# Kernel tuning notes

Measured on AMD Instinct MI355X. Metric: run time of the kernel, lower is better.

Reference implementation:

```python
import jax, jax.numpy as jnp
import numpy as np


def _dwconv(x, w, pad):
    # depthwise conv, NCHW, weight (C,1,kh,kw), feature_group_count=C
    return jax.lax.conv_general_dilated(
        x, w, window_strides=(1, 1), padding=pad,
        feature_group_count=x.shape[1],
        dimension_numbers=('NCHW', 'OIHW', 'NCHW'))


def _max_channel_relu(x):
    # assumed MaxChannelReLU: keep only the channel-max value at each (b,h,w)
    return x * (x == jnp.max(x, axis=1, keepdims=True))


def setup_inputs() -> dict:
    key = jax.random.key(0)
    ks = jax.random.split(key, 6)
    B, C, H, W = 16, 64, 128, 128
    x = jax.random.normal(ks[0], (B, C, H, W), dtype=jnp.float32)
    w_bbx = 0.1 * jax.random.normal(ks[1], (C, 1, 1, 1), dtype=jnp.float32)
    w_width = 0.1 * jax.random.normal(ks[2], (C, 1, 1, 11), dtype=jnp.float32)
    w_width_sh = 0.1 * jax.random.normal(ks[3], (C, 1, 1, 1), dtype=jnp.float32)
    w_height = 0.1 * jax.random.normal(ks[4], (C, 1, 11, 1), dtype=jnp.float32)
    w_height_sh = 0.1 * jax.random.normal(ks[5], (C, 1, 1, 1), dtype=jnp.float32)
    return {"x": x, "w_bbx": w_bbx, "w_width": w_width,
            "w_width_sh": w_width_sh, "w_height": w_height,
            "w_height_sh": w_height_sh}


def reference(x, w_bbx, w_width, w_width_sh, w_height, w_height_sh):
    B, C, H, W = x.shape
    # self.bbx: depthwise 1x1 conv == per-channel scale
    wh = x * w_bbx.reshape(1, C, 1, 1)
    # width branch: depthwise (1,11) conv pad 5, scaled by W, then shared 1x1
    w = _dwconv(wh, w_width, [(0, 0), (5, 5)]) * W
    w = w * w_width_sh.reshape(1, C, 1, 1)
    # height branch: depthwise (11,1) conv pad 5, scaled by H, then shared 1x1
    h = _dwconv(wh, w_height, [(5, 5), (0, 0)]) * H
    h = h * w_height_sh.reshape(1, C, 1, 1)
    sx = jax.nn.sigmoid(x)
    M = jnp.max(sx, axis=(-2, -1), keepdims=True) - 0.01
    score = x * (sx > M).astype(x.dtype)
    S = jnp.sum(score, axis=(-2, -1), keepdims=True)
    sn = score / S  # normalized weights, reused by all weighted reductions
    ws = jnp.sum(w * sn, axis=(-2, -1))
    hs = jnp.sum(h * sn, axis=(-2, -1))
    ps = jnp.max(sx, axis=(-2, -1))
    col = jnp.arange(W, dtype=x.dtype).reshape(1, 1, 1, W)
    row = jnp.arange(H, dtype=x.dtype).reshape(1, 1, H, 1)
    x1 = jnp.sum(col * sn, axis=(-2, -1)) - ws / 2
    y1 = jnp.sum(row * sn, axis=(-2, -1)) - hs / 2
    x2 = x1 + ws
    y2 = y1 + hs
    score_m = _max_channel_relu(score)
    w_m = _max_channel_relu(w)
    h_m = _max_channel_relu(h)
    i = jnp.broadcast_to(jnp.arange(B, dtype=x.dtype)[:, None], (B, C))
    bbox = jnp.stack([i, x1, y1, x2, y2, ps], axis=-1).reshape(-1, 6)
    return jnp.concatenate([score_m, w_m, h_m], axis=1), bbox
```

## Files before the change

kernel.cpp:

```cpp
#include <hip/hip_runtime.h>
#include <math.h>

#define BATCH 16
#define CH    64
#define HH    128
#define WW    128
#define PLANE (HH*WW)
#define OUT0  (BATCH*3*CH*PLANE)
#define SR4    36
#define TSROWS 18
#define PART_OFF 2048
#define MB_OFF   90112
#define MB_N     786432


__device__ __forceinline__ unsigned enc32(float f) {
    unsigned u = __float_as_uint(f);
    return (u & 0x80000000u) ? ~u : (u | 0x80000000u);
}
__device__ __forceinline__ float dec32(unsigned k) {
    unsigned u = (k & 0x80000000u) ? (k ^ 0x80000000u) : ~k;
    return __uint_as_float(u);
}

__global__ __launch_bounds__(256) void k_max(const float* __restrict__ x,
                                             float* __restrict__ ws) {
    int bid = blockIdx.x;
    int tid = threadIdx.x;
    const float4* xp = (const float4*)(x + (size_t)bid * PLANE);
    float m = -INFINITY;
#pragma unroll
    for (int i = 0; i < 16; i++) {
        float4 v = xp[i * 256 + tid];
        m = fmaxf(m, fmaxf(fmaxf(v.x, v.y), fmaxf(v.z, v.w)));
    }
#pragma unroll
    for (int off = 32; off; off >>= 1) m = fmaxf(m, __shfl_xor(m, off, 64));
    __shared__ float sm[4];
    int wid = tid >> 6, lane = tid & 63;
    if (lane == 0) sm[wid] = m;
    __syncthreads();
    if (tid == 0) {
        float mm = fmaxf(fmaxf(sm[0], sm[1]), fmaxf(sm[2], sm[3]));
        float ps = 1.0f / (1.0f + expf(-mm));
        ws[bid] = ps - 0.01f;
        ws[1024 + bid] = ps;
    }
}

template <int CPG>
__global__ __launch_bounds__(256) void k_conv(
    const float* __restrict__ x,
    const float* __restrict__ w_bbx, const float* __restrict__ w_width,
    const float* __restrict__ w_width_sh, const float* __restrict__ w_height,
    const float* __restrict__ w_height_sh,
    const float* __restrict__ ws, float* __restrict__ wsums,
    unsigned long long* __restrict__ mb) {
    __shared__ float4 xs4[2][TSROWS * SR4];
    __shared__ float red[CPG * 4 * 5];
    int t = blockIdx.x;
    int g = blockIdx.y;
    int b = blockIdx.z;
    int tid = threadIdx.x;
    int r = tid >> 5, q = tid & 31;
    int wid = tid >> 6, lane = tid & 63;

    for (int j = tid; j < 2 * TSROWS * SR4; j += 256)
        ((float4*)xs4)[j] = make_float4(0.f, 0.f, 0.f, 0.f);
    __syncthreads();
    int cbase = g * CPG;
    {
        const float* xp = x + (size_t)(b * 64 + cbase) * PLANE;
        for (int j = tid; j < TSROWS * 32; j += 256) {
            int i = j >> 5, c4 = j & 31;
            int gr = t * 8 - 5 + i;
            float4 v = make_float4(0.f, 0.f, 0.f, 0.f);
            if ((unsigned)gr < 128u) v = ((const float4*)xp)[gr * 32 + c4];
            xs4[0][i * SR4 + 2 + c4] = v;
        }
    }
    unsigned long long kW[4], kH[4], kS[4];
#pragma unroll
    for (int j = 0; j < 4; j++) { kW[j] = 0ull; kH[j] = 0ull; kS[j] = 0ull; }

    int cur = 0;
    for (int cc = 0; cc < CPG; cc++) {
        __syncthreads();
        int c = cbase + cc;
        float4 p0 = make_float4(0.f, 0.f, 0.f, 0.f);
        float4 p1 = make_float4(0.f, 0.f, 0.f, 0.f);
        float4 p2 = make_float4(0.f, 0.f, 0.f, 0.f);
        bool have = (cc + 1 < CPG);
        if (have) {
            const float* xp = x + (size_t)(b * 64 + c + 1) * PLANE;
            int i0 = tid >> 5, c4 = tid & 31;
            int g0 = t * 8 - 5 + i0;
            if ((unsigned)g0 < 128u) p0 = ((const float4*)xp)[g0 * 32 + c4];
            int g1 = g0 + 8;
            if ((unsigned)g1 < 128u) p1 = ((const float4*)xp)[g1 * 32 + c4];
            if (tid < 64) {
                int g2 = g0 + 16;
                if ((unsigned)g2 < 128u) p2 = ((const float4*)xp)[g2 * 32 + c4];
            }
        }
        float wkc[11], hkc[11];
#pragma unroll
        for (int k = 0; k < 11; k++) {
            wkc[k] = w_width[c * 11 + k];
            hkc[k] = w_height[c * 11 + k];
        }
        float cb = w_bbx[c];
        float cw = 128.0f * w_width_sh[c] * cb;
        float chs = 128.0f * w_height_sh[c] * cb;
        float M = ws[b * 64 + c];

        float4 vx;
        float hx = 0.f, hy = 0.f, hz = 0.f, hw = 0.f;
#pragma unroll
        for (int k = 0; k < 11; k++) {
            float4 v = xs4[cur][(r + k) * SR4 + 2 + q];
            if (k == 5) vx = v;
            hx += v.x * hkc[k]; hy += v.y * hkc[k];
            hz += v.z * hkc[k]; hw += v.w * hkc[k];
        }
        float wbuf[20];
        {
            float4 a0 = xs4[cur][(r + 5) * SR4 + q + 0];
            float4 a1 = xs4[cur][(r + 5) * SR4 + q + 1];
            float4 a3 = xs4[cur][(r + 5) * SR4 + q + 3];
            float4 a4 = xs4[cur][(r + 5) * SR4 + q + 4];
            wbuf[0] = a0.x;  wbuf[1] = a0.y;  wbuf[2] = a0.z;  wbuf[3] = a0.w;
            wbuf[4] = a1.x;  wbuf[5] = a1.y;  wbuf[6] = a1.z;  wbuf[7] = a1.w;
            wbuf[8] = vx.x;  wbuf[9] = vx.y;  wbuf[10] = vx.z; wbuf[11] = vx.w;
            wbuf[12] = a3.x; wbuf[13] = a3.y; wbuf[14] = a3.z; wbuf[15] = a3.w;
            wbuf[16] = a4.x; wbuf[17] = a4.y; wbuf[18] = a4.z; wbuf[19] = a4.w;
        }
        float wo[4];
#pragma unroll
        for (int j = 0; j < 4; j++) {
            float acc = 0.f;
#pragma unroll
            for (int k = 0; k < 11; k++) acc += wbuf[j + 3 + k] * wkc[k];
            wo[j] = acc * cw;
        }
        float ho[4] = {hx * chs, hy * chs, hz * chs, hw * chs};
        float xv[4] = {vx.x, vx.y, vx.z, vx.w};
        float S = 0.f, Sw = 0.f, Sh = 0.f, Scol = 0.f, Srow = 0.f;
#pragma unroll
        for (int j = 0; j < 4; j++) {
            float sx = 1.0f / (1.0f + expf(-xv[j]));
            float sc = (sx > M) ? xv[j] : 0.0f;
            S += sc;
            Sw += wo[j] * sc;
            Sh += ho[j] * sc;
            Scol += (float)(4 * q + j) * sc;
            unsigned long long cand;
            cand = ((unsigned long long)enc32(sc) << 32) | (unsigned)c;
            if (cand > kS[j]) kS[j] = cand;
            cand = ((unsigned long long)enc32(wo[j]) << 32) | (unsigned)c;
            if (cand > kW[j]) kW[j] = cand;
            cand = ((unsigned long long)enc32(ho[j]) << 32) | (unsigned)c;
            if (cand > kH[j]) kH[j] = cand;
        }
        Srow = (float)(t * 8 + r) * S;
#pragma unroll
        for (int off = 32; off; off >>= 1) {
            S    += __shfl_xor(S, off, 64);
            Sw   += __shfl_xor(Sw, off, 64);
            Sh   += __shfl_xor(Sh, off, 64);
            Scol += __shfl_xor(Scol, off, 64);
            Srow += __shfl_xor(Srow, off, 64);
        }
        if (lane == 0) {
            float* rr = &red[(cc * 4 + wid) * 5];
            rr[0] = S; rr[1] = Sw; rr[2] = Sh; rr[3] = Scol; rr[4] = Srow;
        }
        if (have) {
            int i0 = tid >> 5, c4 = tid & 31;
            xs4[cur ^ 1][i0 * SR4 + 2 + c4] = p0;
            xs4[cur ^ 1][(i0 + 8) * SR4 + 2 + c4] = p1;
            if (tid < 64) xs4[cur ^ 1][(i0 + 16) * SR4 + 2 + c4] = p2;
        }
        cur ^= 1;
    }
    __syncthreads();
    if (tid < CPG * 5) {
        int cc = tid / 5, j = tid % 5;
        float s = red[(cc * 4 + 0) * 5 + j] + red[(cc * 4 + 1) * 5 + j]
                + red[(cc * 4 + 2) * 5 + j] + red[(cc * 4 + 3) * 5 + j];
        int c = cbase + cc;
        wsums[(((size_t)(b * 64 + c)) * 16 + t) * 5 + j] = s;
    }
    int gr = t * 8 + r;
    size_t pix = (size_t)gr * 128 + 4 * q;
    unsigned long long* o = mb + (size_t)g * MB_N;
    size_t i0 = (size_t)(b * 3 + 0) * 16384 + pix;
    size_t i1 = (size_t)(b * 3 + 1) * 16384 + pix;
    size_t i2 = (size_t)(b * 3 + 2) * 16384 + pix;
#pragma unroll
    for (int j = 0; j < 4; j++) {
        o[i0 + j] = kS[j];
        o[i1 + j] = kW[j];
        o[i2 + j] = kH[j];
    }
}

template <int NG>
__global__ __launch_bounds__(256) void k_scatter(
    const unsigned long long* __restrict__ mb, float* __restrict__ out) {
    int chunk = blockIdx.x;
    int f = blockIdx.y;
    int b = blockIdx.z;
    int tid = threadIdx.x;
    size_t pix = (size_t)chunk * 1024 + tid * 4;
    size_t ki = (size_t)(b * 3 + f) * 16384 + pix;
    float val[4];
    int win[4];
#pragma unroll
    for (int j = 0; j < 4; j++) {
        unsigned long long k = 0ull;
#pragma unroll
        for (int g2 = 0; g2 < NG; g2++) {
            unsigned long long kg = mb[(size_t)g2 * MB_N + ki + j];
            if (kg > k) k = kg;
        }
        val[j] = dec32((unsigned)(k >> 32));
        win[j] = (int)(k & 63u);
    }
    float* ob = out + (size_t)(b * 192 + f * 64) * PLANE + pix;
#pragma unroll
    for (int c = 0; c < 64; c++) {
        float4 o;
        o.x = (win[0] == c) ? val[0] : 0.f;
        o.y = (win[1] == c) ? val[1] : 0.f;
        o.z = (win[2] == c) ? val[2] : 0.f;
        o.w = (win[3] == c) ? val[3] : 0.f;
        *(float4*)&ob[(size_t)c * PLANE] = o;
    }
}

__global__ __launch_bounds__(256) void k_bbox(const float* __restrict__ ws,
                                              float* __restrict__ out) {
    int idx = blockIdx.x * 256 + threadIdx.x;
    if (idx >= 1024) return;
    int b = idx >> 6;
    const float* p = ws + PART_OFF + (size_t)idx * 80;
    float S = 0.f, Sw = 0.f, Sh = 0.f, Scol = 0.f, Srow = 0.f;
#pragma unroll
    for (int t = 0; t < 16; t++) {
        S    += p[t * 5 + 0];
        Sw   += p[t * 5 + 1];
        Sh   += p[t * 5 + 2];
        Scol += p[t * 5 + 3];
        Srow += p[t * 5 + 4];
    }
    float ps = ws[1024 + idx];
    float inv = 1.0f / S;
    float wsv = Sw * inv, hsv = Sh * inv;
    float x1 = Scol * inv - 0.5f * wsv;
    float y1 = Srow * inv - 0.5f * hsv;
    float* o = out + OUT0 + (size_t)idx * 6;
    o[0] = (float)b;
    o[1] = x1;
    o[2] = y1;
    o[3] = x1 + wsv;
    o[4] = y1 + hsv;
    o[5] = ps;
}

extern "C" void kernel_launch(void* const* d_in, const int* in_sizes, int n_in,
                              void* d_out, int out_size, void* d_ws, size_t ws_size,
                              hipStream_t stream) {
    const float* x          = (const float*)d_in[0];
    const float* w_bbx      = (const float*)d_in[1];
    const float* w_width    = (const float*)d_in[2];
    const float* w_width_sh = (const float*)d_in[3];
    const float* w_height   = (const float*)d_in[4];
    const float* w_height_sh= (const float*)d_in[5];
    float* out = (float*)d_out;
    float* ws  = (float*)d_ws;
    unsigned long long* mb = (unsigned long long*)(ws + MB_OFF);

    size_t need4 = (size_t)MB_OFF * 4 + 4ull * MB_N * 8ull;

    k_max<<<dim3(1024), dim3(256), 0, stream>>>(x, ws);
    if (ws_size >= need4) {
        k_conv<16><<<dim3(16, 4, 16), dim3(256), 0, stream>>>(
            x, w_bbx, w_width, w_width_sh, w_height, w_height_sh,
            ws, ws + PART_OFF, mb);
        k_scatter<4><<<dim3(16, 3, 16), dim3(256), 0, stream>>>(mb, out);
    } else {
        k_conv<32><<<dim3(16, 2, 16), dim3(256), 0, stream>>>(
            x, w_bbx, w_width, w_width_sh, w_height, w_height_sh,
            ws, ws + PART_OFF, mb);
        k_scatter<2><<<dim3(16, 3, 16), dim3(256), 0, stream>>>(mb, out);
    }
    k_bbox<<<dim3(4), dim3(256), 0, stream>>>(ws, out);
}
```

Before: 348.3 us.

## Use 16-row conv tiles with two rows per thread and XCD-aware block mapping

Adds a k_conv16 kernel in which each block handles 16 output rows instead of 8, and each thread computes two rows. The two rows share their vertical 11-tap loads, which cuts halo overhead and LDS reads per output. Blocks go on a 1-D grid remapped so that neighbouring tiles of the same batch and channel group land on the same XCD, and the scatter stores become nontemporal. The trade-offs are half as many blocks (512), launch_bounds that allow lower occupancy, and more registers per thread.

```diff
diff --git a/kernel.cpp b/kernel.cpp
--- a/kernel.cpp
+++ b/kernel.cpp
@@ -9,9 +9,12 @@
 #define OUT0  (BATCH*3*CH*PLANE)
 #define SR4    36
 #define TSROWS 18
+#define T16R   26
 #define PART_OFF 2048
 #define MB_OFF   90112
 #define MB_N     786432
+
+typedef float f4v __attribute__((ext_vector_type(4)));
 
 
 __device__ __forceinline__ unsigned enc32(float f) {
@@ -48,6 +51,173 @@
     }
 }
 
+__global__ __launch_bounds__(256, 1) void k_conv16(
+    const float* __restrict__ x,
+    const float* __restrict__ w_bbx, const float* __restrict__ w_width,
+    const float* __restrict__ w_width_sh, const float* __restrict__ w_height,
+    const float* __restrict__ w_height_sh,
+    const float* __restrict__ ws, float* __restrict__ wsums,
+    unsigned long long* __restrict__ mb) {
+    __shared__ float4 xs4[2][T16R * SR4];
+    __shared__ float red[16 * 4 * 5];
+    int bid = blockIdx.x;
+    int xcd = bid & 7, kk = (bid >> 3) & 7, t = bid >> 6;
+    int gb = xcd * 8 + kk;
+    int g = gb & 3, b = gb >> 2;
+    int tid = threadIdx.x;
+    int r = tid >> 5, q = tid & 31;
+    int wid = tid >> 6, lane = tid & 63;
+
+    for (int j = tid; j < 2 * T16R * SR4; j += 256)
+        ((float4*)xs4)[j] = make_float4(0.f, 0.f, 0.f, 0.f);
+    __syncthreads();
+    int cbase = g * 16;
+    {
+        const float* xp = x + (size_t)(b * 64 + cbase) * PLANE;
+        for (int j = tid; j < T16R * 32; j += 256) {
+            int i = j >> 5, c4 = j & 31;
+            int gr = t * 16 - 5 + i;
+            float4 v = make_float4(0.f, 0.f, 0.f, 0.f);
+            if ((unsigned)gr < 128u) v = ((const float4*)xp)[gr * 32 + c4];
+            xs4[0][i * SR4 + 2 + c4] = v;
+        }
+    }
+    unsigned long long kS[2][4], kW[2][4], kH[2][4];
+#pragma unroll
+    for (int rr = 0; rr < 2; rr++)
+#pragma unroll
+        for (int j = 0; j < 4; j++) { kS[rr][j] = 0; kW[rr][j] = 0; kH[rr][j] = 0; }
+
+    int cur = 0;
+    for (int cc = 0; cc < 16; cc++) {
+        __syncthreads();
+        int c = cbase + cc;
+        float4 p0 = make_float4(0,0,0,0), p1 = p0, p2 = p0, p3 = p0;
+        bool have = (cc + 1 < 16);
+        int i0 = tid >> 5, c4 = tid & 31;
+        if (have) {
+            const float* xp = x + (size_t)(b * 64 + c + 1) * PLANE;
+            int gr0 = t * 16 - 5 + i0;
+            if ((unsigned)gr0 < 128u) p0 = ((const float4*)xp)[gr0 * 32 + c4];
+            int gr1 = gr0 + 8;
+            if ((unsigned)gr1 < 128u) p1 = ((const float4*)xp)[gr1 * 32 + c4];
+            int gr2 = gr0 + 16;
+            if ((unsigned)gr2 < 128u) p2 = ((const float4*)xp)[gr2 * 32 + c4];
+            if (tid < 64) {
+                int gr3 = gr0 + 24;
+                if ((unsigned)gr3 < 128u) p3 = ((const float4*)xp)[gr3 * 32 + c4];
+            }
+        }
+        float wkc[11], hkc[11];
+#pragma unroll
+        for (int k = 0; k < 11; k++) {
+            wkc[k] = w_width[c * 11 + k];
+            hkc[k] = w_height[c * 11 + k];
+        }
+        float cb = w_bbx[c];
+        float cw = 128.0f * w_width_sh[c] * cb;
+        float chs = 128.0f * w_height_sh[c] * cb;
+        float M = ws[b * 64 + c];
+
+        float a0x=0,a0y=0,a0z=0,a0w=0, a1x=0,a1y=0,a1z=0,a1w=0;
+        float4 vx0, vx1;
+#pragma unroll
+        for (int k = 0; k < 12; k++) {
+            float4 v = xs4[cur][(2 * r + k) * SR4 + 2 + q];
+            if (k == 5) vx0 = v;
+            if (k == 6) vx1 = v;
+            if (k < 11) {
+                float h = hkc[k];
+                a0x += v.x*h; a0y += v.y*h; a0z += v.z*h; a0w += v.w*h;
+            }
+            if (k >= 1) {
+                float h = hkc[k-1];
+                a1x += v.x*h; a1y += v.y*h; a1z += v.z*h; a1w += v.w*h;
+            }
+        }
+        float ho[2][4] = {{a0x*chs, a0y*chs, a0z*chs, a0w*chs},
+                          {a1x*chs, a1y*chs, a1z*chs, a1w*chs}};
+        float S = 0.f, Sw = 0.f, Sh = 0.f, Scol = 0.f, Srow = 0.f;
+#pragma unroll
+        for (int rr = 0; rr < 2; rr++) {
+            float4 vc = (rr == 0) ? vx0 : vx1;
+            int srow = (2 * r + 5 + rr) * SR4 + q;
+            float4 b0 = xs4[cur][srow + 0];
+            float4 b1 = xs4[cur][srow + 1];
+            float4 b3 = xs4[cur][srow + 3];
+            float4 b4 = xs4[cur][srow + 4];
+            float wbuf[20] = {b0.x,b0.y,b0.z,b0.w, b1.x,b1.y,b1.z,b1.w,
+                              vc.x,vc.y,vc.z,vc.w, b3.x,b3.y,b3.z,b3.w,
+                              b4.x,b4.y,b4.z,b4.w};
+            float xv[4] = {vc.x, vc.y, vc.z, vc.w};
+            float s4 = 0.f;
+#pragma unroll
+            for (int j = 0; j < 4; j++) {
+                float acc = 0.f;
+#pragma unroll
+                for (int k = 0; k < 11; k++) acc += wbuf[j + 3 + k] * wkc[k];
+                float wo = acc * cw;
+                float sx = 1.0f / (1.0f + expf(-xv[j]));
+                float sc = (sx > M) ? xv[j] : 0.0f;
+                s4 += sc;
+                Sw += wo * sc;
+                Sh += ho[rr][j] * sc;
+                Scol += (float)(4 * q + j) * sc;
+                unsigned long long cand;
+                cand = ((unsigned long long)enc32(sc) << 32) | (unsigned)c;
+                if (cand > kS[rr][j]) kS[rr][j] = cand;
+                cand = ((unsigned long long)enc32(wo) << 32) | (unsigned)c;
+                if (cand > kW[rr][j]) kW[rr][j] = cand;
+                cand = ((unsigned long long)enc32(ho[rr][j]) << 32) | (unsigned)c;
+                if (cand > kH[rr][j]) kH[rr][j] = cand;
+            }
+            S += s4;
+            Srow += (float)(t * 16 + 2 * r + rr) * s4;
+        }
+#pragma unroll
+        for (int off = 32; off; off >>= 1) {
+            S    += __shfl_xor(S, off, 64);
+            Sw   += __shfl_xor(Sw, off, 64);
+            Sh   += __shfl_xor(Sh, off, 64);
+            Scol += __shfl_xor(Scol, off, 64);
+            Srow += __shfl_xor(Srow, off, 64);
+        }
+        if (lane == 0) {
+            float* rr2 = &red[(cc * 4 + wid) * 5];
+            rr2[0] = S; rr2[1] = Sw; rr2[2] = Sh; rr2[3] = Scol; rr2[4] = Srow;
+        }
+        if (have) {
+            xs4[cur ^ 1][i0 * SR4 + 2 + c4] = p0;
+            xs4[cur ^ 1][(i0 + 8) * SR4 + 2 + c4] = p1;
+            xs4[cur ^ 1][(i0 + 16) * SR4 + 2 + c4] = p2;
+            if (tid < 64) xs4[cur ^ 1][(i0 + 24) * SR4 + 2 + c4] = p3;
+        }
+        cur ^= 1;
+    }
+    __syncthreads();
+    if (tid < 80) {
+        int cc = tid / 5, j = tid % 5;
+        float s = red[(cc * 4 + 0) * 5 + j] + red[(cc * 4 + 1) * 5 + j]
+                + red[(cc * 4 + 2) * 5 + j] + red[(cc * 4 + 3) * 5 + j];
+        int c = cbase + cc;
+        wsums[(((size_t)(b * 64 + c)) * 8 + t) * 5 + j] = s;
+    }
+    int y0 = t * 16 + 2 * r;
+    size_t pix = (size_t)y0 * 128 + 4 * q;
+    unsigned long long* o = mb + (size_t)g * MB_N;
+    size_t i0s = (size_t)(b * 3 + 0) * 16384 + pix;
+    size_t i1s = (size_t)(b * 3 + 1) * 16384 + pix;
+    size_t i2s = (size_t)(b * 3 + 2) * 16384 + pix;
+#pragma unroll
+    for (int rr = 0; rr < 2; rr++)
+#pragma unroll
+        for (int j = 0; j < 4; j++) {
+            o[i0s + rr * 128 + j] = kS[rr][j];
+            o[i1s + rr * 128 + j] = kW[rr][j];
+            o[i2s + rr * 128 + j] = kH[rr][j];
+        }
+}
+
 template <int CPG>
 __global__ __launch_bounds__(256) void k_conv(
     const float* __restrict__ x,
@@ -58,13 +228,10 @@
     unsigned long long* __restrict__ mb) {
     __shared__ float4 xs4[2][TSROWS * SR4];
     __shared__ float red[CPG * 4 * 5];
-    int t = blockIdx.x;
-    int g = blockIdx.y;
-    int b = blockIdx.z;
+    int t = blockIdx.x, g = blockIdx.y, b = blockIdx.z;
     int tid = threadIdx.x;
     int r = tid >> 5, q = tid & 31;
     int wid = tid >> 6, lane = tid & 63;
-
     for (int j = tid; j < 2 * TSROWS * SR4; j += 256)
         ((float4*)xs4)[j] = make_float4(0.f, 0.f, 0.f, 0.f);
     __syncthreads();
@@ -82,14 +249,11 @@
     unsigned long long kW[4], kH[4], kS[4];
 #pragma unroll
     for (int j = 0; j < 4; j++) { kW[j] = 0ull; kH[j] = 0ull; kS[j] = 0ull; }
-
     int cur = 0;
     for (int cc = 0; cc < CPG; cc++) {
         __syncthreads();
         int c = cbase + cc;
-        float4 p0 = make_float4(0.f, 0.f, 0.f, 0.f);
-        float4 p1 = make_float4(0.f, 0.f, 0.f, 0.f);
-        float4 p2 = make_float4(0.f, 0.f, 0.f, 0.f);
+        float4 p0 = make_float4(0,0,0,0), p1 = p0, p2 = p0;
         bool have = (cc + 1 < CPG);
         if (have) {
             const float* xp = x + (size_t)(b * 64 + c + 1) * PLANE;
@@ -113,7 +277,6 @@
         float cw = 128.0f * w_width_sh[c] * cb;
         float chs = 128.0f * w_height_sh[c] * cb;
         float M = ws[b * 64 + c];
-
         float4 vx;
         float hx = 0.f, hy = 0.f, hz = 0.f, hw = 0.f;
 #pragma unroll
@@ -129,11 +292,11 @@
             float4 a1 = xs4[cur][(r + 5) * SR4 + q + 1];
             float4 a3 = xs4[cur][(r + 5) * SR4 + q + 3];
             float4 a4 = xs4[cur][(r + 5) * SR4 + q + 4];
-            wbuf[0] = a0.x;  wbuf[1] = a0.y;  wbuf[2] = a0.z;  wbuf[3] = a0.w;
-            wbuf[4] = a1.x;  wbuf[5] = a1.y;  wbuf[6] = a1.z;  wbuf[7] = a1.w;
-            wbuf[8] = vx.x;  wbuf[9] = vx.y;  wbuf[10] = vx.z; wbuf[11] = vx.w;
-            wbuf[12] = a3.x; wbuf[13] = a3.y; wbuf[14] = a3.z; wbuf[15] = a3.w;
-            wbuf[16] = a4.x; wbuf[17] = a4.y; wbuf[18] = a4.z; wbuf[19] = a4.w;
+            wbuf[0]=a0.x; wbuf[1]=a0.y; wbuf[2]=a0.z; wbuf[3]=a0.w;
+            wbuf[4]=a1.x; wbuf[5]=a1.y; wbuf[6]=a1.z; wbuf[7]=a1.w;
+            wbuf[8]=vx.x; wbuf[9]=vx.y; wbuf[10]=vx.z; wbuf[11]=vx.w;
+            wbuf[12]=a3.x; wbuf[13]=a3.y; wbuf[14]=a3.z; wbuf[15]=a3.w;
+            wbuf[16]=a4.x; wbuf[17]=a4.y; wbuf[18]=a4.z; wbuf[19]=a4.w;
         }
         float wo[4];
 #pragma unroll
@@ -150,9 +313,7 @@
         for (int j = 0; j < 4; j++) {
             float sx = 1.0f / (1.0f + expf(-xv[j]));
             float sc = (sx > M) ? xv[j] : 0.0f;
-            S += sc;
-            Sw += wo[j] * sc;
-            Sh += ho[j] * sc;
+            S += sc; Sw += wo[j] * sc; Sh += ho[j] * sc;
             Scol += (float)(4 * q + j) * sc;
             unsigned long long cand;
             cand = ((unsigned long long)enc32(sc) << 32) | (unsigned)c;
@@ -230,24 +391,25 @@
     float* ob = out + (size_t)(b * 192 + f * 64) * PLANE + pix;
 #pragma unroll
     for (int c = 0; c < 64; c++) {
-        float4 o;
+        f4v o;
         o.x = (win[0] == c) ? val[0] : 0.f;
         o.y = (win[1] == c) ? val[1] : 0.f;
         o.z = (win[2] == c) ? val[2] : 0.f;
         o.w = (win[3] == c) ? val[3] : 0.f;
-        *(float4*)&ob[(size_t)c * PLANE] = o;
-    }
-}
-
+        __builtin_nontemporal_store(o, (f4v*)&ob[(size_t)c * PLANE]);
+    }
+}
+
+template <int NT>
 __global__ __launch_bounds__(256) void k_bbox(const float* __restrict__ ws,
                                               float* __restrict__ out) {
     int idx = blockIdx.x * 256 + threadIdx.x;
     if (idx >= 1024) return;
     int b = idx >> 6;
-    const float* p = ws + PART_OFF + (size_t)idx * 80;
+    const float* p = ws + PART_OFF + (size_t)idx * (NT * 5);
     float S = 0.f, Sw = 0.f, Sh = 0.f, Scol = 0.f, Srow = 0.f;
 #pragma unroll
-    for (int t = 0; t < 16; t++) {
+    for (int t = 0; t < NT; t++) {
         S    += p[t * 5 + 0];
         Sw   += p[t * 5 + 1];
         Sh   += p[t * 5 + 2];
@@ -285,15 +447,16 @@
 
     k_max<<<dim3(1024), dim3(256), 0, stream>>>(x, ws);
     if (ws_size >= need4) {
-        k_conv<16><<<dim3(16, 4, 16), dim3(256), 0, stream>>>(
+        k_conv16<<<dim3(512), dim3(256), 0, stream>>>(
             x, w_bbx, w_width, w_width_sh, w_height, w_height_sh,
             ws, ws + PART_OFF, mb);
         k_scatter<4><<<dim3(16, 3, 16), dim3(256), 0, stream>>>(mb, out);
+        k_bbox<8><<<dim3(4), dim3(256), 0, stream>>>(ws, out);
     } else {
         k_conv<32><<<dim3(16, 2, 16), dim3(256), 0, stream>>>(
             x, w_bbx, w_width, w_width_sh, w_height, w_height_sh,
             ws, ws + PART_OFF, mb);
         k_scatter<2><<<dim3(16, 3, 16), dim3(256), 0, stream>>>(mb, out);
-    }
-    k_bbox<<<dim3(4), dim3(256), 0, stream>>>(ws, out);
-}
+        k_bbox<16><<<dim3(4), dim3(256), 0, stream>>>(ws, out);
+    }
+}
```

After: 338.0 us. 2.9% less time.
